# Performance work log

Measured on AMD Instinct MI355X. Metric: run time of the kernel, lower is better.

The kernel has to match this reference:

```python
import math
import jax, jax.numpy as jnp
import numpy as np

B, S, D, H = 4, 2048, 768, 8


def setup_inputs() -> dict:
    key = jax.random.key(0)
    ks = jax.random.split(key, 8)
    x = jax.random.normal(ks[0], (B, S, D), dtype=jnp.float32)
    # padding mask: True = masked position, shape [B, S, 1] as consumed by forward
    attention_mask = jax.random.randint(ks[1], (B, S, 1), 0, 2) == 1
    W_q = jax.random.normal(ks[2], (D, D), dtype=jnp.float32) * 0.02
    b_q = jax.random.normal(ks[3], (D,), dtype=jnp.float32) * 0.02
    W_v = jax.random.normal(ks[4], (D, D), dtype=jnp.float32) * 0.02
    b_v = jax.random.normal(ks[5], (D,), dtype=jnp.float32) * 0.02
    gamma = jnp.ones((D,), dtype=jnp.float32)
    beta = jnp.zeros((D,), dtype=jnp.float32)
    return {"x": x, "attention_mask": attention_mask, "W_q": W_q, "b_q": b_q,
            "W_v": W_v, "b_v": b_v, "gamma": gamma, "beta": beta}


def reference(x, attention_mask, W_q, b_q, W_v, b_v, gamma, beta):
    b, s, d = x.shape
    dk = d // H
    scale = math.sqrt(dk)
    q = (x @ W_q.T + b_q).reshape(b, s, H, dk).transpose(0, 2, 1, 3)  # [B,H,S,dk]
    # faithful to source: k and v BOTH use the V projection (original bug)
    kv = (x @ W_v.T + b_v).reshape(b, s, H, dk).transpose(0, 2, 1, 3)
    k = kv
    v = kv
    weight = jnp.einsum('bhid,bhjd->bhij', q, k) / scale  # [B,H,S,S]
    pad = attention_mask[:, None, :, :]                   # [B,1,S,1] -> broadcast over heads, j
    causal = jnp.triu(jnp.ones((s, s), dtype=bool), 1)    # [S,S]
    mask = pad | causal
    weight = jnp.where(mask, jnp.float32(-1e9), weight)
    # faithful: softmax over dim=2 (the query axis), as in the source
    score = jax.nn.softmax(weight, axis=2)
    out = jnp.einsum('bhij,bhjd->bhid', score, v)         # [B,H,S,dk]
    out = out.transpose(0, 2, 1, 3).reshape(b, s, d)
    out = out + x                                          # residual
    mu = jnp.mean(out, axis=-1, keepdims=True)
    var = jnp.mean((out - mu) ** 2, axis=-1, keepdims=True)
    return (out - mu) / jnp.sqrt(var + 1e-5) * gamma + beta
```

## Files before the change

kernel.cpp:

```cpp
#include <hip/hip_runtime.h>

#define B 4
#define S 2048
#define D 768
#define H 8
#define DK 96
#define NBH (B*H)
#define SD (B*S*D)

typedef __bf16 bf16x8 __attribute__((ext_vector_type(8)));
typedef float f32x4 __attribute__((ext_vector_type(4)));
typedef unsigned short ushort_t;
typedef __attribute__((ext_vector_type(8))) unsigned short ushort8;
typedef __attribute__((ext_vector_type(4))) unsigned short us4;

static constexpr float NEG = -1.0e9f;
static constexpr float SCALE_L2E = 0.14724515567714155f;

__device__ __forceinline__ float exp2v(float x) { return __builtin_amdgcn_exp2f(x); }

__device__ __forceinline__ ushort_t f2bf(float f) {
    union { float f; unsigned u; } v; v.f = f;
    unsigned r = v.u + 0x7fffu + ((v.u >> 16) & 1u);
    return (ushort_t)(r >> 16);
}

__device__ __forceinline__ unsigned cvt_pk(float a, float b) {
    unsigned d;
    asm("v_cvt_pk_bf16_f32 %0, %1, %2" : "=v"(d) : "v"(a), "v"(b));
    return d;
}
__device__ __forceinline__ ushort8 pack8(const float4& a, const float4& b) {
    union { unsigned u[4]; ushort8 s; } r;
    r.u[0] = cvt_pk(a.x, a.y); r.u[1] = cvt_pk(a.z, a.w);
    r.u[2] = cvt_pk(b.x, b.y); r.u[3] = cvt_pk(b.z, b.w);
    return r.s;
}
__device__ __forceinline__ us4 pack4(const float4& a) {
    union { unsigned u[2]; us4 s; } r;
    r.u[0] = cvt_pk(a.x, a.y); r.u[1] = cvt_pk(a.z, a.w);
    return r.s;
}

#define MFMA16(a, b, c) __builtin_amdgcn_mfma_f32_16x16x32_bf16((a), (b), (c), 0, 0, 0)

__global__ __launch_bounds__(256) void convert_bf16(
    const float* __restrict__ wq, const float* __restrict__ wv,
    ushort_t* __restrict__ wqb, ushort_t* __restrict__ wvb)
{
    const int stride = gridDim.x * 256;
    const int idx = blockIdx.x * 256 + threadIdx.x;
    for (int i = idx; i < (D * D) / 4; i += stride) {
        ((us4*)wqb)[i] = pack4(((const float4*)wq)[i]);
        ((us4*)wvb)[i] = pack4(((const float4*)wv)[i]);
    }
}

__global__ __launch_bounds__(256) void in_proj_gemm(
    const float* __restrict__ x,
    const ushort_t* __restrict__ wqb, const float* __restrict__ bq,
    const ushort_t* __restrict__ wvb, const float* __restrict__ bv,
    ushort_t* __restrict__ Qb, ushort_t* __restrict__ KVb,
    ushort_t* __restrict__ KVt)
{
    const ushort_t* __restrict__ Wm = blockIdx.z ? wvb : wqb;
    const float* __restrict__ bia   = blockIdx.z ? bv : bq;
    ushort_t* __restrict__ outp     = blockIdx.z ? KVb : Qb;
    const float osc = blockIdx.z ? 1.0f : SCALE_L2E;

    const int bn = blockIdx.x * 128;
    const int bm = blockIdx.y * 128;
    const int tid = threadIdx.x;
    const int lane = tid & 63;
    const int wid = tid >> 6;
    const int wm = (wid >> 1) * 64, wn = (wid & 1) * 64;
    const int lr = lane & 15, lg = lane >> 4;

    __shared__ __align__(16) ushort_t As[2][128][40];
    __shared__ __align__(16) ushort_t Bs[2][128][40];

    const int r0 = tid >> 2, c8 = (tid & 3) * 8;
    const float*    xg0 = &x [(size_t)(bm + r0) * D + c8];
    const float*    xg1 = xg0 + (size_t)64 * D;
    const ushort_t* wg0 = &Wm[(size_t)(bn + r0) * D + c8];
    const ushort_t* wg1 = wg0 + (size_t)64 * D;

    float4 xv[4];
    ushort8 wv2[2];

    f32x4 acc[4][4];
    #pragma unroll
    for (int m = 0; m < 4; ++m)
        #pragma unroll
        for (int n = 0; n < 4; ++n) acc[m][n] = (f32x4){0.f, 0.f, 0.f, 0.f};

    {
        xv[0] = *(const float4*)(xg0);     xv[1] = *(const float4*)(xg0 + 4);
        xv[2] = *(const float4*)(xg1);     xv[3] = *(const float4*)(xg1 + 4);
        wv2[0] = *(const ushort8*)(wg0);   wv2[1] = *(const ushort8*)(wg1);
        *(ushort8*)&As[0][r0][c8]      = pack8(xv[0], xv[1]);
        *(ushort8*)&As[0][r0 + 64][c8] = pack8(xv[2], xv[3]);
        *(ushort8*)&Bs[0][r0][c8]      = wv2[0];
        *(ushort8*)&Bs[0][r0 + 64][c8] = wv2[1];
    }

    for (int k = 0; k < 24; ++k) {
        __syncthreads();
        const int buf = k & 1;
        if (k < 23) {
            const int ko = (k + 1) * 32;
            xv[0] = *(const float4*)(xg0 + ko);     xv[1] = *(const float4*)(xg0 + ko + 4);
            xv[2] = *(const float4*)(xg1 + ko);     xv[3] = *(const float4*)(xg1 + ko + 4);
            wv2[0] = *(const ushort8*)(wg0 + ko);   wv2[1] = *(const ushort8*)(wg1 + ko);
        }
        bf16x8 a[4], bfr[4];
        #pragma unroll
        for (int m = 0; m < 4; ++m) a[m]   = *(const bf16x8*)&As[buf][wm + m * 16 + lr][lg * 8];
        #pragma unroll
        for (int n = 0; n < 4; ++n) bfr[n] = *(const bf16x8*)&Bs[buf][wn + n * 16 + lr][lg * 8];
        #pragma unroll
        for (int m = 0; m < 4; ++m)
            #pragma unroll
            for (int n = 0; n < 4; ++n)
                acc[m][n] = MFMA16(a[m], bfr[n], acc[m][n]);
        if (k < 23) {
            const int nb = (k + 1) & 1;
            *(ushort8*)&As[nb][r0][c8]      = pack8(xv[0], xv[1]);
            *(ushort8*)&As[nb][r0 + 64][c8] = pack8(xv[2], xv[3]);
            *(ushort8*)&Bs[nb][r0][c8]      = wv2[0];
            *(ushort8*)&Bs[nb][r0 + 64][c8] = wv2[1];
        }
    }

    #pragma unroll
    for (int m = 0; m < 4; ++m) {
        #pragma unroll
        for (int n = 0; n < 4; ++n) {
            int col = bn + wn + n * 16 + lr;
            float bb = bia[col];
            int row0 = bm + wm + m * 16 + lg * 4;
            us4 o;
            #pragma unroll
            for (int r = 0; r < 4; ++r) o[r] = f2bf((acc[m][n][r] + bb) * osc);
            #pragma unroll
            for (int r = 0; r < 4; ++r) outp[(size_t)(row0 + r) * D + col] = o[r];
            if (blockIdx.z) {
                int hh = col / DK, dd = col - hh * DK;
                int bb2 = row0 >> 11, ss = row0 & (S - 1);
                *(us4*)&KVt[((size_t)(bb2 * H + hh) * DK + dd) * S + ss] = o;
            }
        }
    }
}

__global__ __launch_bounds__(256) void col_stats(
    const ushort_t* __restrict__ Qb, const ushort_t* __restrict__ KVb,
    const int* __restrict__ amask,
    float* __restrict__ colM, float* __restrict__ colSinv)
{
    const int bh = blockIdx.y;
    const int jt = (bh & 16) ? (31 - (int)blockIdx.x) : (int)blockIdx.x;
    const int b = bh >> 3, h = bh & 7;
    const int j0 = jt * 64;
    const int tid = threadIdx.x;
    const int lane = tid & 63;
    const int w = tid >> 6;
    const int lr = lane & 15, lg = lane >> 4;

    __shared__ __align__(16) ushort_t qs[2][64][104];
    __shared__ int pads[2][64];

    bf16x8 kf[3];
    #pragma unroll
    for (int ks2 = 0; ks2 < 3; ++ks2)
        kf[ks2] = *(const bf16x8*)&KVb[(size_t)(b * S + j0 + w * 16 + lr) * D + h * DK + ks2 * 32 + lg * 8];

    int kr[3], kc[3];
    const ushort_t* qg[3];
    #pragma unroll
    for (int k3 = 0; k3 < 3; ++k3) {
        int c = tid + k3 * 256;
        kr[k3] = c / 12; kc[k3] = (c % 12) * 8;
        qg[k3] = &Qb[(size_t)(b * S + j0 + kr[k3]) * D + h * DK + kc[k3]];
    }
    const int* pg = amask + b * S + j0 + (tid < 64 ? tid : 0);

    ushort8 pq[3]; int ppad = 0;
    #pragma unroll
    for (int k3 = 0; k3 < 3; ++k3) { pq[k3] = *(const ushort8*)qg[k3]; qg[k3] += (size_t)64 * D; }
    if (tid < 64) { ppad = *pg; }
    pg += 64;

    float m = NEG, ssum = 0.f;
    const int jg = j0 + w * 16 + lr;
    const int nit = (S / 64) - jt;

    for (int t = 0; t < nit; ++t) {
        const int buf = t & 1;
        const int i0 = j0 + t * 64;
        #pragma unroll
        for (int k3 = 0; k3 < 3; ++k3) *(ushort8*)&qs[buf][kr[k3]][kc[k3]] = pq[k3];
        if (tid < 64) pads[buf][tid] = ppad;
        __syncthreads();
        if (t + 1 < nit) {
            #pragma unroll
            for (int k3 = 0; k3 < 3; ++k3) { pq[k3] = *(const ushort8*)qg[k3]; qg[k3] += (size_t)64 * D; }
            if (tid < 64) { ppad = *pg; }
            pg += 64;
        }

        f32x4 dacc[4];
        #pragma unroll
        for (int f = 0; f < 4; ++f) dacc[f] = (f32x4){0.f, 0.f, 0.f, 0.f};
        #pragma unroll
        for (int ks2 = 0; ks2 < 3; ++ks2) {
            #pragma unroll
            for (int f = 0; f < 4; ++f) {
                bf16x8 afr = *(const bf16x8*)&qs[buf][f * 16 + lr][ks2 * 32 + lg * 8];
                dacc[f] = MFMA16(afr, kf[ks2], dacc[f]);
            }
        }

        #pragma unroll
        for (int f = 0; f < 4; ++f) {
            const int ib = f * 16 + lg * 4;
            float wv[4];
            #pragma unroll
            for (int r = 0; r < 4; ++r) {
                int ig = i0 + ib + r;
                wv[r] = (pads[buf][ib + r] != 0 || jg > ig) ? NEG : dacc[f][r];
            }
            float vmax = fmaxf(fmaxf(wv[0], wv[1]), fmaxf(wv[2], wv[3]));
            float mn = fmaxf(m, vmax);
            ssum = ssum * exp2v(m - mn)
                 + exp2v(wv[0] - mn) + exp2v(wv[1] - mn)
                 + exp2v(wv[2] - mn) + exp2v(wv[3] - mn);
            m = mn;
        }
    }

    float m2 = m, s2 = ssum;
    #pragma unroll
    for (int off = 16; off < 64; off <<= 1) {
        float mo = __shfl_xor(m2, off);
        float so = __shfl_xor(s2, off);
        float mn = fmaxf(m2, mo);
        s2 = s2 * exp2v(m2 - mn) + so * exp2v(mo - mn);
        m2 = mn;
    }
    if (lane < 16) {
        if (m2 == NEG) s2 += (float)j0;
        colM[bh * S + jg] = m2;
        colSinv[bh * S + jg] = 1.0f / s2;
    }
}

__global__ __launch_bounds__(512, 4) void attn_pv(
    const ushort_t* __restrict__ Qb, const ushort_t* __restrict__ KVb,
    const ushort_t* __restrict__ KVt,
    const int* __restrict__ amask,
    const float* __restrict__ colM, const float* __restrict__ colSinv,
    const float* __restrict__ x, float* __restrict__ out)
{
    const int bh = blockIdx.y;
    const int it = (bh & 16) ? (15 - (int)blockIdx.x) : (int)blockIdx.x;
    const int b = bh >> 3, h = bh & 7;
    const int i0 = it * 128;
    const int tid = threadIdx.x;
    const int lane = tid & 63;
    const int w = tid >> 6;
    const int lr = lane & 15, lg = lane >> 4;

    __shared__ __align__(16) ushort_t kvs[64][104];
    __shared__ __align__(16) ushort_t kvt[96][88];
    __shared__ __align__(16) ushort_t ps[128][72];
    __shared__ __align__(16) float cm[64];
    __shared__ __align__(16) float csv[64];

    bf16x8 qf[3];
    #pragma unroll
    for (int ks2 = 0; ks2 < 3; ++ks2)
        qf[ks2] = *(const bf16x8*)&Qb[(size_t)(b * S + i0 + w * 16 + lr) * D + h * DK + ks2 * 32 + lg * 8];

    const int my_pad = (int)(amask[b * S + i0 + w * 16 + lr] != 0);
    const int i_g = i0 + w * 16 + lr;

    ushort_t* ldst[3];
    const ushort_t* gsrc[3];
    size_t gstr[3];
    #pragma unroll
    for (int k3 = 0; k3 < 3; ++k3) {
        int c = tid + k3 * 512;
        if (c < 768) {
            int r = c / 12, cc = (c % 12) * 8;
            ldst[k3] = &kvs[r][cc];
            gsrc[k3] = &KVb[(size_t)(b * S + r) * D + h * DK + cc];
            gstr[k3] = (size_t)64 * D;
        } else {
            int c2 = c - 768;
            int r = c2 >> 3, cc = (c2 & 7) * 8;
            ldst[k3] = &kvt[r][cc];
            gsrc[k3] = &KVt[((size_t)(b * H + h) * DK + r) * S + cc];
            gstr[k3] = 64;
        }
    }
    const float* cmg  = colM    + (size_t)bh * S + (tid < 64 ? tid : 0);
    const float* csvg = colSinv + (size_t)bh * S + (tid < 64 ? tid : 0);

    ushort8 pk[3]; float pcm = 0.f, pcsv = 0.f;
    #pragma unroll
    for (int k3 = 0; k3 < 3; ++k3) { pk[k3] = *(const ushort8*)gsrc[k3]; gsrc[k3] += gstr[k3]; }
    if (tid < 64) { pcm = *cmg; pcsv = *csvg; }
    cmg += 64; csvg += 64;

    f32x4 acc[6];
    #pragma unroll
    for (int df = 0; df < 6; ++df) acc[df] = (f32x4){0.f, 0.f, 0.f, 0.f};

    const int nj = 2 * it + 2;
    for (int jt2 = 0; jt2 < nj; ++jt2) {
        const int j0 = jt2 * 64;
        __syncthreads();
        #pragma unroll
        for (int k3 = 0; k3 < 3; ++k3)
            *(ushort8*)ldst[k3] = pk[k3];
        if (tid < 64) { cm[tid] = pcm; csv[tid] = pcsv; }
        __syncthreads();
        if (jt2 + 1 < nj) {
            #pragma unroll
            for (int k3 = 0; k3 < 3; ++k3) { pk[k3] = *(const ushort8*)gsrc[k3]; gsrc[k3] += gstr[k3]; }
            if (tid < 64) { pcm = *cmg; pcsv = *csvg; }
            cmg += 64; csvg += 64;
        }

        f32x4 dacc[4];
        #pragma unroll
        for (int jf = 0; jf < 4; ++jf) dacc[jf] = (f32x4){0.f, 0.f, 0.f, 0.f};
        #pragma unroll
        for (int ks2 = 0; ks2 < 3; ++ks2) {
            #pragma unroll
            for (int jf = 0; jf < 4; ++jf) {
                bf16x8 bfr = *(const bf16x8*)&kvs[jf * 16 + lr][ks2 * 32 + lg * 8];
                dacc[jf] = MFMA16(bfr, qf[ks2], dacc[jf]);
            }
        }

        #pragma unroll
        for (int jf = 0; jf < 4; ++jf) {
            const int jbase = jf * 16 + lg * 4;
            f32x4 cmv  = *(const f32x4*)&cm[jbase];
            f32x4 csvv = *(const f32x4*)&csv[jbase];
            float pv[4];
            #pragma unroll
            for (int r = 0; r < 4; ++r) {
                int jgl = j0 + jbase + r;
                bool msk = my_pad || (jgl > i_g);
                float wvv = msk ? NEG : dacc[jf][r];
                pv[r] = exp2v(wvv - cmv[r]) * csvv[r];
            }
            union { unsigned u[2]; uint2 v; } o;
            o.u[0] = cvt_pk(pv[0], pv[1]);
            o.u[1] = cvt_pk(pv[2], pv[3]);
            *(uint2*)&ps[w * 16 + lr][jbase] = o.v;
        }

        #pragma unroll
        for (int ks2 = 0; ks2 < 2; ++ks2) {
            bf16x8 afr = *(const bf16x8*)&ps[w * 16 + lr][ks2 * 32 + lg * 8];
            #pragma unroll
            for (int df = 0; df < 6; ++df) {
                bf16x8 bfr = *(const bf16x8*)&kvt[df * 16 + lr][ks2 * 32 + lg * 8];
                acc[df] = MFMA16(afr, bfr, acc[df]);
            }
        }
    }

    #pragma unroll
    for (int df = 0; df < 6; ++df) {
        int d = h * DK + df * 16 + lr;
        #pragma unroll
        for (int r = 0; r < 4; ++r) {
            size_t gi = (size_t)(b * S + i0 + w * 16 + lg * 4 + r) * D + d;
            out[gi] = acc[df][r] + x[gi];
        }
    }
}

__global__ __launch_bounds__(256) void layer_norm(
    float* __restrict__ out,
    const float* __restrict__ gamma, const float* __restrict__ beta)
{
    const int row = blockIdx.x * 4 + (threadIdx.x >> 6);
    const int lane = threadIdx.x & 63;
    float* o = out + (size_t)row * D;

    float4 v[3];
    #pragma unroll
    for (int p = 0; p < 3; ++p) v[p] = *(const float4*)&o[lane * 4 + p * 256];

    float s = 0.f;
    #pragma unroll
    for (int p = 0; p < 3; ++p) s += v[p].x + v[p].y + v[p].z + v[p].w;
    #pragma unroll
    for (int off = 1; off < 64; off <<= 1) s += __shfl_xor(s, off);
    const float mu = s * (1.0f / D);

    float q = 0.f;
    #pragma unroll
    for (int p = 0; p < 3; ++p) {
        float a = v[p].x - mu, bb = v[p].y - mu, c = v[p].z - mu, dd = v[p].w - mu;
        q += a * a + bb * bb + c * c + dd * dd;
    }
    #pragma unroll
    for (int off = 1; off < 64; off <<= 1) q += __shfl_xor(q, off);
    const float inv = 1.0f / sqrtf(q * (1.0f / D) + 1e-5f);

    #pragma unroll
    for (int p = 0; p < 3; ++p) {
        float4 g = *(const float4*)&gamma[lane * 4 + p * 256];
        float4 bt = *(const float4*)&beta[lane * 4 + p * 256];
        float4 r;
        r.x = (v[p].x - mu) * inv * g.x + bt.x;
        r.y = (v[p].y - mu) * inv * g.y + bt.y;
        r.z = (v[p].z - mu) * inv * g.z + bt.z;
        r.w = (v[p].w - mu) * inv * g.w + bt.w;
        *(float4*)&o[lane * 4 + p * 256] = r;
    }
}

extern "C" void kernel_launch(void* const* d_in, const int* in_sizes, int n_in,
                              void* d_out, int out_size, void* d_ws, size_t ws_size,
                              hipStream_t stream)
{
    const float* x     = (const float*)d_in[0];
    const int*   amask = (const int*)  d_in[1];
    const float* Wq    = (const float*)d_in[2];
    const float* bq    = (const float*)d_in[3];
    const float* Wv    = (const float*)d_in[4];
    const float* bv    = (const float*)d_in[5];
    const float* gamma = (const float*)d_in[6];
    const float* beta  = (const float*)d_in[7];
    float* out = (float*)d_out;

    ushort_t* wqb  = (ushort_t*)d_ws;
    ushort_t* wvb  = wqb + (size_t)D * D;
    ushort_t* Qb   = wvb + (size_t)D * D;
    ushort_t* KVb  = Qb  + (size_t)SD;
    ushort_t* KVt  = KVb + (size_t)SD;
    float* colM    = (float*)(KVt + (size_t)SD);
    float* colSinv = colM + (size_t)NBH * S;

    convert_bf16<<<576, 256, 0, stream>>>(Wq, Wv, wqb, wvb);
    in_proj_gemm<<<dim3(D / 128, (B * S) / 128, 2), 256, 0, stream>>>(
        x, wqb, bq, wvb, bv, Qb, KVb, KVt);
    col_stats<<<dim3(S / 64, NBH), 256, 0, stream>>>(
        Qb, KVb, amask, colM, colSinv);
    attn_pv<<<dim3(16, 32), 512, 0, stream>>>(
        Qb, KVb, KVt, amask, colM, colSinv, x, out);
    layer_norm<<<(B * S) / 4, 256, 0, stream>>>(out, gamma, beta);
}
```

Measured before the change: 158.5 us.

## Fuse weight bf16 conversion into GEMM and widen col_stats blocks to 128 columns

Removes the separate convert_bf16 kernel, so the projection GEMM now loads fp32 weights and packs them to bf16 while staging into shared memory. This saves one launch and a workspace round trip, but each GEMM block now reads twice the weight bytes. col_stats now uses 512-thread blocks, each covering 128 key columns across 8 waves. That halves the number of blocks and lets the loaded Q tiles be reused across twice as many columns.

```diff
diff --git a/kernel.cpp b/kernel.cpp
--- a/kernel.cpp
+++ b/kernel.cpp
@@ -36,36 +36,19 @@
     r.u[2] = cvt_pk(b.x, b.y); r.u[3] = cvt_pk(b.z, b.w);
     return r.s;
 }
-__device__ __forceinline__ us4 pack4(const float4& a) {
-    union { unsigned u[2]; us4 s; } r;
-    r.u[0] = cvt_pk(a.x, a.y); r.u[1] = cvt_pk(a.z, a.w);
-    return r.s;
-}
 
 #define MFMA16(a, b, c) __builtin_amdgcn_mfma_f32_16x16x32_bf16((a), (b), (c), 0, 0, 0)
-
-__global__ __launch_bounds__(256) void convert_bf16(
-    const float* __restrict__ wq, const float* __restrict__ wv,
-    ushort_t* __restrict__ wqb, ushort_t* __restrict__ wvb)
-{
-    const int stride = gridDim.x * 256;
-    const int idx = blockIdx.x * 256 + threadIdx.x;
-    for (int i = idx; i < (D * D) / 4; i += stride) {
-        ((us4*)wqb)[i] = pack4(((const float4*)wq)[i]);
-        ((us4*)wvb)[i] = pack4(((const float4*)wv)[i]);
-    }
-}
 
 __global__ __launch_bounds__(256) void in_proj_gemm(
     const float* __restrict__ x,
-    const ushort_t* __restrict__ wqb, const float* __restrict__ bq,
-    const ushort_t* __restrict__ wvb, const float* __restrict__ bv,
+    const float* __restrict__ Wq, const float* __restrict__ bq,
+    const float* __restrict__ Wv, const float* __restrict__ bv,
     ushort_t* __restrict__ Qb, ushort_t* __restrict__ KVb,
     ushort_t* __restrict__ KVt)
 {
-    const ushort_t* __restrict__ Wm = blockIdx.z ? wvb : wqb;
-    const float* __restrict__ bia   = blockIdx.z ? bv : bq;
-    ushort_t* __restrict__ outp     = blockIdx.z ? KVb : Qb;
+    const float* __restrict__ Wm  = blockIdx.z ? Wv : Wq;
+    const float* __restrict__ bia = blockIdx.z ? bv : bq;
+    ushort_t* __restrict__ outp   = blockIdx.z ? KVb : Qb;
     const float osc = blockIdx.z ? 1.0f : SCALE_L2E;
 
     const int bn = blockIdx.x * 128;
@@ -80,13 +63,12 @@
     __shared__ __align__(16) ushort_t Bs[2][128][40];
 
     const int r0 = tid >> 2, c8 = (tid & 3) * 8;
-    const float*    xg0 = &x [(size_t)(bm + r0) * D + c8];
-    const float*    xg1 = xg0 + (size_t)64 * D;
-    const ushort_t* wg0 = &Wm[(size_t)(bn + r0) * D + c8];
-    const ushort_t* wg1 = wg0 + (size_t)64 * D;
-
-    float4 xv[4];
-    ushort8 wv2[2];
+    const float* xg0 = &x [(size_t)(bm + r0) * D + c8];
+    const float* xg1 = xg0 + (size_t)64 * D;
+    const float* wg0 = &Wm[(size_t)(bn + r0) * D + c8];
+    const float* wg1 = wg0 + (size_t)64 * D;
+
+    float4 xv[4], wv4[4];
 
     f32x4 acc[4][4];
     #pragma unroll
@@ -95,13 +77,14 @@
         for (int n = 0; n < 4; ++n) acc[m][n] = (f32x4){0.f, 0.f, 0.f, 0.f};
 
     {
-        xv[0] = *(const float4*)(xg0);     xv[1] = *(const float4*)(xg0 + 4);
-        xv[2] = *(const float4*)(xg1);     xv[3] = *(const float4*)(xg1 + 4);
-        wv2[0] = *(const ushort8*)(wg0);   wv2[1] = *(const ushort8*)(wg1);
+        xv[0] = *(const float4*)(xg0);      xv[1] = *(const float4*)(xg0 + 4);
+        xv[2] = *(const float4*)(xg1);      xv[3] = *(const float4*)(xg1 + 4);
+        wv4[0] = *(const float4*)(wg0);     wv4[1] = *(const float4*)(wg0 + 4);
+        wv4[2] = *(const float4*)(wg1);     wv4[3] = *(const float4*)(wg1 + 4);
         *(ushort8*)&As[0][r0][c8]      = pack8(xv[0], xv[1]);
         *(ushort8*)&As[0][r0 + 64][c8] = pack8(xv[2], xv[3]);
-        *(ushort8*)&Bs[0][r0][c8]      = wv2[0];
-        *(ushort8*)&Bs[0][r0 + 64][c8] = wv2[1];
+        *(ushort8*)&Bs[0][r0][c8]      = pack8(wv4[0], wv4[1]);
+        *(ushort8*)&Bs[0][r0 + 64][c8] = pack8(wv4[2], wv4[3]);
     }
 
     for (int k = 0; k < 24; ++k) {
@@ -109,9 +92,10 @@
         const int buf = k & 1;
         if (k < 23) {
             const int ko = (k + 1) * 32;
-            xv[0] = *(const float4*)(xg0 + ko);     xv[1] = *(const float4*)(xg0 + ko + 4);
-            xv[2] = *(const float4*)(xg1 + ko);     xv[3] = *(const float4*)(xg1 + ko + 4);
-            wv2[0] = *(const ushort8*)(wg0 + ko);   wv2[1] = *(const ushort8*)(wg1 + ko);
+            xv[0] = *(const float4*)(xg0 + ko);      xv[1] = *(const float4*)(xg0 + ko + 4);
+            xv[2] = *(const float4*)(xg1 + ko);      xv[3] = *(const float4*)(xg1 + ko + 4);
+            wv4[0] = *(const float4*)(wg0 + ko);     wv4[1] = *(const float4*)(wg0 + ko + 4);
+            wv4[2] = *(const float4*)(wg1 + ko);     wv4[3] = *(const float4*)(wg1 + ko + 4);
         }
         bf16x8 a[4], bfr[4];
         #pragma unroll
@@ -127,8 +111,8 @@
             const int nb = (k + 1) & 1;
             *(ushort8*)&As[nb][r0][c8]      = pack8(xv[0], xv[1]);
             *(ushort8*)&As[nb][r0 + 64][c8] = pack8(xv[2], xv[3]);
-            *(ushort8*)&Bs[nb][r0][c8]      = wv2[0];
-            *(ushort8*)&Bs[nb][r0 + 64][c8] = wv2[1];
+            *(ushort8*)&Bs[nb][r0][c8]      = pack8(wv4[0], wv4[1]);
+            *(ushort8*)&Bs[nb][r0 + 64][c8] = pack8(wv4[2], wv4[3]);
         }
     }
 
@@ -153,15 +137,15 @@
     }
 }
 
-__global__ __launch_bounds__(256) void col_stats(
+__global__ __launch_bounds__(512) void col_stats(
     const ushort_t* __restrict__ Qb, const ushort_t* __restrict__ KVb,
     const int* __restrict__ amask,
     float* __restrict__ colM, float* __restrict__ colSinv)
 {
     const int bh = blockIdx.y;
-    const int jt = (bh & 16) ? (31 - (int)blockIdx.x) : (int)blockIdx.x;
+    const int jt = (bh & 16) ? (15 - (int)blockIdx.x) : (int)blockIdx.x;
     const int b = bh >> 3, h = bh & 7;
-    const int j0 = jt * 64;
+    const int j0 = jt * 128;
     const int tid = threadIdx.x;
     const int lane = tid & 63;
     const int w = tid >> 6;
@@ -175,36 +159,34 @@
     for (int ks2 = 0; ks2 < 3; ++ks2)
         kf[ks2] = *(const bf16x8*)&KVb[(size_t)(b * S + j0 + w * 16 + lr) * D + h * DK + ks2 * 32 + lg * 8];
 
-    int kr[3], kc[3];
-    const ushort_t* qg[3];
-    #pragma unroll
-    for (int k3 = 0; k3 < 3; ++k3) {
-        int c = tid + k3 * 256;
-        kr[k3] = c / 12; kc[k3] = (c % 12) * 8;
-        qg[k3] = &Qb[(size_t)(b * S + j0 + kr[k3]) * D + h * DK + kc[k3]];
-    }
+    const bool v1 = tid < 256;
+    const int c0 = tid, c1 = tid + 512;
+    const int kr0 = c0 / 12, kc0 = (c0 % 12) * 8;
+    const int kr1 = (c1 < 768) ? c1 / 12 : 0, kc1 = (c1 < 768) ? (c1 % 12) * 8 : 0;
+    const ushort_t* qg0 = &Qb[(size_t)(b * S + j0 + kr0) * D + h * DK + kc0];
+    const ushort_t* qg1 = &Qb[(size_t)(b * S + j0 + kr1) * D + h * DK + kc1];
     const int* pg = amask + b * S + j0 + (tid < 64 ? tid : 0);
 
-    ushort8 pq[3]; int ppad = 0;
-    #pragma unroll
-    for (int k3 = 0; k3 < 3; ++k3) { pq[k3] = *(const ushort8*)qg[k3]; qg[k3] += (size_t)64 * D; }
+    ushort8 pq0, pq1; int ppad = 0;
+    pq0 = *(const ushort8*)qg0; qg0 += (size_t)64 * D;
+    if (v1) { pq1 = *(const ushort8*)qg1; } qg1 += (size_t)64 * D;
     if (tid < 64) { ppad = *pg; }
     pg += 64;
 
     float m = NEG, ssum = 0.f;
     const int jg = j0 + w * 16 + lr;
-    const int nit = (S / 64) - jt;
+    const int nit = 32 - 2 * jt;
 
     for (int t = 0; t < nit; ++t) {
         const int buf = t & 1;
         const int i0 = j0 + t * 64;
-        #pragma unroll
-        for (int k3 = 0; k3 < 3; ++k3) *(ushort8*)&qs[buf][kr[k3]][kc[k3]] = pq[k3];
+        *(ushort8*)&qs[buf][kr0][kc0] = pq0;
+        if (v1) *(ushort8*)&qs[buf][kr1][kc1] = pq1;
         if (tid < 64) pads[buf][tid] = ppad;
         __syncthreads();
         if (t + 1 < nit) {
-            #pragma unroll
-            for (int k3 = 0; k3 < 3; ++k3) { pq[k3] = *(const ushort8*)qg[k3]; qg[k3] += (size_t)64 * D; }
+            pq0 = *(const ushort8*)qg0; qg0 += (size_t)64 * D;
+            if (v1) { pq1 = *(const ushort8*)qg1; } qg1 += (size_t)64 * D;
             if (tid < 64) { ppad = *pg; }
             pg += 64;
         }
@@ -442,18 +424,15 @@
     const float* beta  = (const float*)d_in[7];
     float* out = (float*)d_out;
 
-    ushort_t* wqb  = (ushort_t*)d_ws;
-    ushort_t* wvb  = wqb + (size_t)D * D;
-    ushort_t* Qb   = wvb + (size_t)D * D;
+    ushort_t* Qb   = (ushort_t*)d_ws;
     ushort_t* KVb  = Qb  + (size_t)SD;
     ushort_t* KVt  = KVb + (size_t)SD;
     float* colM    = (float*)(KVt + (size_t)SD);
     float* colSinv = colM + (size_t)NBH * S;
 
-    convert_bf16<<<576, 256, 0, stream>>>(Wq, Wv, wqb, wvb);
     in_proj_gemm<<<dim3(D / 128, (B * S) / 128, 2), 256, 0, stream>>>(
-        x, wqb, bq, wvb, bv, Qb, KVb, KVt);
-    col_stats<<<dim3(S / 64, NBH), 256, 0, stream>>>(
+        x, Wq, bq, Wv, bv, Qb, KVb, KVt);
+    col_stats<<<dim3(16, NBH), 512, 0, stream>>>(
         Qb, KVb, amask, colM, colSinv);
     attn_pv<<<dim3(16, 32), 512, 0, stream>>>(
         Qb, KVb, KVt, amask, colM, colSinv, x, out);
```

New measurement: 161.0 us. About the same (+1.6%).
